# Performance work log

Hardware: AMD Instinct MI355X
Metric: run time of the kernel (lower is better)

Reference implementation:

```python
import jax, jax.numpy as jnp
import numpy as np

B, C, H, W = 8, 512, 32, 32
NH = 8
DH = C // NH
HW = H * W
LN_EPS = 1e-5
NORM_EPS = 1e-12  # torch F.normalize eps


def setup_inputs() -> dict:
    key = jax.random.key(0)
    ks = jax.random.split(key, 8)
    s = 0.02
    return {
        "x": jax.random.normal(ks[0], (B, C, H, W), dtype=jnp.float32),
        "qkv_w": jax.random.normal(ks[1], (3 * C, C), dtype=jnp.float32) * s,
        "proj_w": jax.random.normal(ks[2], (C, C), dtype=jnp.float32) * s,
        "proj_b": jnp.zeros((C,), dtype=jnp.float32),
        "temperature": jnp.ones((NH, 1, 1), dtype=jnp.float32),
        "ln_g": jnp.ones((C,), dtype=jnp.float32),
        "ln_b": jnp.zeros((C,), dtype=jnp.float32),
        "pos_embed": jax.random.normal(ks[3], (1, HW, C), dtype=jnp.float32) * s,
        "dw_w": jax.random.normal(ks[4], (C, 1, 3, 3), dtype=jnp.float32) * s,
        "dw_b": jnp.zeros((C,), dtype=jnp.float32),
        "pw_w": jax.random.normal(ks[5], (C, C, 1, 1), dtype=jnp.float32) * s,
        "pw_b": jnp.zeros((C,), dtype=jnp.float32),
    }


def _l2norm_tokens(t):
    # normalize along token axis (dim=-2), like F.normalize(t, dim=-2)
    n = jnp.sqrt(jnp.sum(t * t, axis=-2, keepdims=True))
    return t / jnp.maximum(n, NORM_EPS)


def _layernorm(t, g, b):
    mu = jnp.mean(t, axis=-1, keepdims=True)
    var = jnp.mean((t - mu) ** 2, axis=-1, keepdims=True)
    return (t - mu) * jax.lax.rsqrt(var + LN_EPS) * g + b


def _dsconv(t, dw_w, dw_b, pw_w, pw_b):
    # depthwise 3x3 SAME + pointwise 1x1, NCHW / OIHW
    y = jax.lax.conv_general_dilated(
        t, dw_w, window_strides=(1, 1), padding="SAME",
        dimension_numbers=("NCHW", "OIHW", "NCHW"), feature_group_count=C)
    y = y + dw_b[None, :, None, None]
    y = jax.lax.conv_general_dilated(
        y, pw_w, window_strides=(1, 1), padding="SAME",
        dimension_numbers=("NCHW", "OIHW", "NCHW"))
    return y + pw_b[None, :, None, None]


def reference(x, qkv_w, proj_w, proj_b, temperature, ln_g, ln_b, pos_embed, dw_w, dw_b, pw_w, pw_b):
    save = x
    t = jnp.transpose(x.reshape(B, C, HW), (0, 2, 1))  # [B, HW, C]
    t = t + pos_embed
    # qkv projection (no bias)
    qkv = t @ qkv_w.T  # [B, HW, 3C]
    qkv = qkv.reshape(B, HW, 3, NH, DH).transpose(2, 0, 3, 1, 4)  # [3,B,NH,HW,DH]
    q, k, v = qkv[0], qkv[1], qkv[2]
    q = _l2norm_tokens(q)
    k = _l2norm_tokens(k)
    attn = jnp.einsum("bhnd,bhmd->bhnm", q, k) * temperature[None]  # [B,NH,HW,HW]
    attn = jax.nn.softmax(attn, axis=-1)
    o = jnp.einsum("bhnm,bhmd->bhnd", attn, v)  # [B,NH,HW,DH]
    o = o.transpose(0, 2, 1, 3).reshape(B, HW, C)
    o = o @ proj_w.T + proj_b
    o = _layernorm(o, ln_g, ln_b)
    o = jnp.transpose(o, (0, 2, 1)).reshape(B, C, H, W)
    o = o + save
    return o + _dsconv(o, dw_w, dw_b, pw_w, pw_b)
```

## Files before the change

### kernel.cpp

```cpp
#include <hip/hip_runtime.h>
#include <math.h>

#define BB_ 8
#define C_ 512
#define C3_ 1536
#define HW_ 1024
#define NH_ 8
#define DH_ 64
#define HH_ 32
#define WW_ 32

typedef __attribute__((ext_vector_type(8))) short short8;
typedef __attribute__((ext_vector_type(4))) short short4v;
typedef __attribute__((ext_vector_type(8))) unsigned short ushort8;
typedef __attribute__((ext_vector_type(4))) unsigned short ushort4_t;
typedef __attribute__((ext_vector_type(4))) float f32x4;
typedef unsigned short ushort;

__device__ inline ushort f2bf(float f) {
  union { float f; unsigned u; } v;
  v.f = f;
  unsigned r = v.u + 0x7fffu + ((v.u >> 16) & 1u);
  return (ushort)(r >> 16);
}
__device__ inline float bf2f(ushort u) {
  union { unsigned u; float f; } v;
  v.u = ((unsigned)u) << 16;
  return v.f;
}

__device__ inline unsigned cvt_pk_bf16(float a, float b) {
  unsigned r;
  asm("v_cvt_pk_bf16_f32 %0, %1, %2" : "=v"(r) : "v"(a), "v"(b));
  return r;
}

__device__ inline float fast_exp2(float x) {
#if __has_builtin(__builtin_amdgcn_exp2f)
  return __builtin_amdgcn_exp2f(x);
#else
  return exp2f(x);
#endif
}

#define GLD16(gptr, lptr)                                                     \
  __builtin_amdgcn_global_load_lds(                                           \
      (const __attribute__((address_space(1))) unsigned int*)(gptr),          \
      (__attribute__((address_space(3))) unsigned int*)(lptr), 16, 0, 0)

__global__ __launch_bounds__(256) void prep_kernel(
    const float* __restrict__ x, const float* __restrict__ pos,
    const float* __restrict__ qkv_w, const float* __restrict__ proj_w,
    const float* __restrict__ pw_w, ushort* __restrict__ t,
    ushort* __restrict__ xT, ushort* __restrict__ wts,
    float* __restrict__ sums) {
  const int bid = blockIdx.x;
  const int tid = threadIdx.x;
  if (bid >= 2304) {
    sums[(bid - 2304) * 256 + tid] = 0.f;
    return;
  }
  if (bid >= 1024) {
    int i = ((bid - 1024) * 256 + tid) * 4;
    float4 v;
    if (i < 786432) v = *(const float4*)&qkv_w[i];
    else if (i < 1048576) v = *(const float4*)&proj_w[i - 786432];
    else v = *(const float4*)&pw_w[i - 1048576];
    union { unsigned u[2]; ushort4_t s; } o4;
    o4.u[0] = cvt_pk_bf16(v.x, v.y);
    o4.u[1] = cvt_pk_bf16(v.z, v.w);
    *(ushort4_t*)&wts[i] = o4.s;
    return;
  }
  __shared__ float tile[64][65];
  const int n0 = (bid & 15) * 64, c0 = ((bid >> 4) & 7) * 64, b = bid >> 7;
#pragma unroll
  for (int it = 0; it < 4; it++) {
    int c_l = (tid >> 4) + it * 16;
    int n_l4 = (tid & 15) * 4;
    float4 v = *(const float4*)&x[((size_t)(b * C_ + c0 + c_l)) * HW_ + n0 + n_l4];
    tile[c_l][n_l4 + 0] = v.x;
    tile[c_l][n_l4 + 1] = v.y;
    tile[c_l][n_l4 + 2] = v.z;
    tile[c_l][n_l4 + 3] = v.w;
  }
  __syncthreads();
#pragma unroll
  for (int it = 0; it < 4; it++) {
    int n_l = (tid >> 4) + it * 16;
    int c_l4 = (tid & 15) * 4;
    size_t token = (size_t)(b * HW_ + n0 + n_l);
    float4 pv = *(const float4*)&pos[(n0 + n_l) * C_ + c0 + c_l4];
    float xv0 = tile[c_l4 + 0][n_l], xv1 = tile[c_l4 + 1][n_l];
    float xv2 = tile[c_l4 + 2][n_l], xv3 = tile[c_l4 + 3][n_l];
    ushort4_t tb = {f2bf(xv0 + pv.x), f2bf(xv1 + pv.y), f2bf(xv2 + pv.z),
                    f2bf(xv3 + pv.w)};
    ushort4_t xb = {f2bf(xv0), f2bf(xv1), f2bf(xv2), f2bf(xv3)};
    *(ushort4_t*)&t[token * C_ + c0 + c_l4] = tb;
    *(ushort4_t*)&xT[token * C_ + c0 + c_l4] = xb;
  }
}

__global__ __launch_bounds__(256) void gemm_qkv(
    const ushort* __restrict__ A, const ushort* __restrict__ Wm,
    ushort* __restrict__ out, ushort* __restrict__ vt,
    float* __restrict__ qsum, float* __restrict__ ksum) {
  const int N = C3_, K = C_;
  __shared__ alignas(16) ushort smem[2 * 128 * 64];
  ushort* As = smem;
  ushort* Bs = smem + 128 * 64;
  const int f = blockIdx.y * gridDim.x + blockIdx.x;
  const int xcd = f & 7, idx = f >> 3;
  const int bm = (xcd * 8 + idx / 12) * 128;
  const int bn = (idx % 12) * 128;
  const int tid = threadIdx.x;
  const int w = tid >> 6, lane = tid & 63;
  const int wm = 64 * (w & 1), wn = 64 * (w >> 1);
  const int l15 = lane & 15, lq = lane >> 4;

  f32x4 acc[4][4];
#pragma unroll
  for (int i = 0; i < 4; i++)
#pragma unroll
    for (int j = 0; j < 4; j++) acc[i][j] = (f32x4){0.f, 0.f, 0.f, 0.f};

  const int srr8 = lane >> 3, sq3 = lane & 7;

  for (int k0 = 0; k0 < K; k0 += 64) {
    __syncthreads();
#pragma unroll
    for (int it = 0; it < 4; it++) {
      int r = w * 32 + it * 8 + srr8;
      int g = (sq3 - r) & 7;
      GLD16(A + (size_t)(bm + r) * K + k0 + g * 8, &As[(w * 32 + it * 8) * 64]);
      GLD16(Wm + (size_t)(bn + r) * K + k0 + g * 8, &Bs[(w * 32 + it * 8) * 64]);
    }
    __syncthreads();
#pragma unroll
    for (int kk = 0; kk < 2; kk++) {
      short8 af[4], bf[4];
#pragma unroll
      for (int nt = 0; nt < 4; nt++) {
        int r = wm + nt * 16 + l15;
        af[nt] = *(const short8*)&As[r * 64 + (((kk * 4 + lq) + r) & 7) * 8];
        int c = wn + nt * 16 + l15;
        bf[nt] = *(const short8*)&Bs[c * 64 + (((kk * 4 + lq) + c) & 7) * 8];
      }
#pragma unroll
      for (int i = 0; i < 4; i++)
#pragma unroll
        for (int j = 0; j < 4; j++)
          acc[i][j] = __builtin_amdgcn_mfma_f32_16x16x32_bf16(
              af[i], bf[j], acc[i][j], 0, 0, 0);
    }
  }

  const int b = bm >> 10;
  if (bn < 1024) {
    __syncthreads();
    ushort* T = smem;
#pragma unroll
    for (int j = 0; j < 4; j++) {
      int c_l = wn + j * 16 + l15;
      int c = bn + c_l;
      float ss = 0.f;
#pragma unroll
      for (int i = 0; i < 4; i++) {
#pragma unroll
        for (int r = 0; r < 4; r++) {
          int m_l = wm + i * 16 + lq * 4 + r;
          float v = acc[i][j][r];
          ss += v * v;
          T[m_l * 128 + (((c_l >> 3) ^ (m_l & 15)) << 3) + (c_l & 7)] =
              f2bf(v);
        }
      }
      ss += __shfl_xor(ss, 16);
      ss += __shfl_xor(ss, 32);
      if (lq == 0) {
        if (c < 512) atomicAdd(&qsum[b * 512 + c], ss);
        else atomicAdd(&ksum[b * 512 + c - 512], ss);
      }
    }
    __syncthreads();
    const int jj = tid & 15, mrow = tid >> 4;
#pragma unroll
    for (int p = 0; p < 8; p++) {
      int m_l = p * 16 + mrow;
      ushort8 v8 = *(const ushort8*)&T[m_l * 128 + ((jj ^ (m_l & 15)) << 3)];
      *(ushort8*)&out[(size_t)(bm + m_l) * N + bn + jj * 8] = v8;
    }
  } else {
    __syncthreads();
    ushort* T = smem;
#pragma unroll
    for (int j = 0; j < 4; j++) {
      int c_l = wn + j * 16 + l15;
#pragma unroll
      for (int i = 0; i < 4; i++) {
        int n_l = wm + i * 16 + lq * 4;
        union { unsigned u[2]; ushort4_t s; } pu;
        pu.u[0] = cvt_pk_bf16(acc[i][j][0], acc[i][j][1]);
        pu.u[1] = cvt_pk_bf16(acc[i][j][2], acc[i][j][3]);
        *(ushort4_t*)&T[c_l * 128 + (((n_l >> 3) ^ (c_l & 15)) << 3) +
                        (n_l & 7)] = pu.s;
      }
    }
    __syncthreads();
    const int jj = tid & 15, crow = tid >> 4;
    const int n0 = bm & 1023;
#pragma unroll
    for (int p = 0; p < 8; p++) {
      int c_l = p * 16 + crow;
      ushort8 v8 = *(const ushort8*)&T[c_l * 128 + ((jj ^ (c_l & 15)) << 3)];
      int hd = bn - 1024 + c_l;
      *(ushort8*)&vt[((size_t)(b * 512 + hd)) * HW_ + n0 + jj * 8] = v8;
    }
  }
}

template <int EPI>
__global__ __launch_bounds__(256) void gemm_n64(
    const ushort* __restrict__ A, const ushort* __restrict__ Wm,
    const float* __restrict__ bias, void* __restrict__ outv,
    const ushort* __restrict__ resid, int N, int K) {
  __shared__ alignas(16) ushort As[128 * 64];
  __shared__ alignas(16) ushort Bs[64 * 64];
  __shared__ alignas(16) float Cs[EPI == 2 ? 64 * 128 : 4];
  const int f = blockIdx.y * gridDim.x + blockIdx.x;
  const int xcd = f & 7, idx = f >> 3;
  const int nbx = gridDim.x;
  const int bm = (xcd * (gridDim.y >> 3) + idx / nbx) * 128;
  const int bn = (idx % nbx) * 64;
  const int tid = threadIdx.x;
  const int w = tid >> 6, lane = tid & 63;
  const int wm = 64 * (w & 1), wn = 32 * (w >> 1);
  const int l15 = lane & 15, lq = lane >> 4;

  f32x4 acc[4][2];
#pragma unroll
  for (int i = 0; i < 4; i++)
#pragma unroll
    for (int j = 0; j < 2; j++) acc[i][j] = (f32x4){0.f, 0.f, 0.f, 0.f};

  const int srr8 = lane >> 3, sq3 = lane & 7;

  for (int k0 = 0; k0 < K; k0 += 64) {
    __syncthreads();
#pragma unroll
    for (int it = 0; it < 4; it++) {
      int r = w * 32 + it * 8 + srr8;
      int g = (sq3 - r) & 7;
      GLD16(A + (size_t)(bm + r) * K + k0 + g * 8, &As[(w * 32 + it * 8) * 64]);
    }
#pragma unroll
    for (int it = 0; it < 2; it++) {
      int r = w * 16 + it * 8 + srr8;
      int g = (sq3 - r) & 7;
      GLD16(Wm + (size_t)(bn + r) * K + k0 + g * 8, &Bs[(w * 16 + it * 8) * 64]);
    }
    __syncthreads();
#pragma unroll
    for (int kk = 0; kk < 2; kk++) {
      short8 af[4], bf[2];
#pragma unroll
      for (int nt = 0; nt < 4; nt++) {
        int r = wm + nt * 16 + l15;
        af[nt] = *(const short8*)&As[r * 64 + (((kk * 4 + lq) + r) & 7) * 8];
      }
#pragma unroll
      for (int j = 0; j < 2; j++) {
        int c = wn + j * 16 + l15;
        bf[j] = *(const short8*)&Bs[c * 64 + (((kk * 4 + lq) + c) & 7) * 8];
      }
#pragma unroll
      for (int i = 0; i < 4; i++)
#pragma unroll
        for (int j = 0; j < 2; j++)
          acc[i][j] = __builtin_amdgcn_mfma_f32_16x16x32_bf16(
              af[i], bf[j], acc[i][j], 0, 0, 0);
    }
  }

  if (EPI == 1) {
#pragma unroll
    for (int i = 0; i < 4; i++) {
#pragma unroll
      for (int j = 0; j < 2; j++) {
        int c = bn + wn + j * 16 + l15;
        float bv = bias[c];
#pragma unroll
        for (int r = 0; r < 4; r++) {
          int m = bm + wm + i * 16 + lq * 4 + r;
          float v = acc[i][j][r] + bv;
          ((ushort*)outv)[(size_t)m * N + c] = f2bf(v);
        }
      }
    }
  } else {
#pragma unroll
    for (int i = 0; i < 4; i++) {
#pragma unroll
      for (int j = 0; j < 2; j++) {
        int c_l = wn + j * 16 + l15;
        int m_l = wm + i * 16 + lq * 4;
        float bv = bias[bn + c_l];
        f32x4 vv;
#pragma unroll
        for (int r = 0; r < 4; r++) {
          int m = bm + m_l + r;
          vv[r] = acc[i][j][r] + bv + bf2f(resid[(size_t)m * C_ + bn + c_l]);
        }
        int phys = (m_l >> 2) ^ (c_l & 31);
        *(f32x4*)&Cs[c_l * 128 + phys * 4] = vv;
      }
    }
    __syncthreads();
    const int b = bm >> 10, s0 = bm & (HW_ - 1);
    const int l5 = tid & 31;
    const int rr = tid >> 5;
    float* outp = (float*)outv;
#pragma unroll
    for (int pass = 0; pass < 8; pass++) {
      int row = rr + pass * 8;
      int phys = l5 ^ (row & 31);
      f32x4 vv = *(const f32x4*)&Cs[row * 128 + phys * 4];
      *(f32x4*)&outp[((size_t)(b * C_ + bn + row)) * HW_ + s0 + l5 * 4] = vv;
    }
  }
}

__global__ __launch_bounds__(256) void attn_mfma_kernel(
    const ushort* __restrict__ qkv, const ushort* __restrict__ vt,
    const float* __restrict__ qsum, const float* __restrict__ ksum,
    const float* __restrict__ temp, ushort* __restrict__ o) {
  __shared__ alignas(16) ushort Ks[2][64 * 64];
  __shared__ alignas(16) ushort Vts[2][64 * 64];
  __shared__ float sc_lds[64];

  const int tid = threadIdx.x;
  const int w = tid >> 6, lane = tid & 63;
  const int quad = lane >> 4, lcol = lane & 15;
  const int bh = blockIdx.x & 63;
  const int qt = blockIdx.x >> 6;
  const int b = bh >> 3, h = bh & 7;
  const int q0 = qt * 128;

  if (tid < 64) {
    float qs = qsum[b * 512 + h * 64 + tid];
    float ks = ksum[b * 512 + h * 64 + tid];
    float iq = 1.0f / fmaxf(sqrtf(qs), 1e-12f);
    float ik = 1.0f / fmaxf(sqrtf(ks), 1e-12f);
    sc_lds[tid] = iq * ik * temp[h] * 1.44269504088896340736f;
  }

  const ushort* kg = qkv + (size_t)b * HW_ * C3_ + C_ + h * 64;
  const ushort* vg = vt + (size_t)(bh * 64) * HW_;

  const int srow0 = tid >> 3;
  const int sc = tid & 7;

#pragma unroll
  for (int it = 0; it < 2; it++) {
    int row = srow0 + it * 32;
    int scg = sc ^ (row & 7);
    GLD16(kg + (size_t)row * C3_ + scg * 8, &Ks[0][w * 512 + it * 2048]);
    GLD16(vg + (size_t)row * HW_ + scg * 8, &Vts[0][w * 512 + it * 2048]);
  }
  __syncthreads();

  short8 qf[2][2];
#pragma unroll
  for (int qg = 0; qg < 2; qg++) {
    const int m = q0 + w * 32 + qg * 16 + lcol;
    const ushort* qrow = qkv + ((size_t)(b * HW_ + m)) * C3_ + h * 64;
#pragma unroll
    for (int kc = 0; kc < 2; kc++) {
      ushort8 q8 = *(const ushort8*)&qrow[kc * 32 + quad * 8];
      union { short8 v; ushort u[8]; } pk;
#pragma unroll
      for (int j = 0; j < 8; j++) {
        int d = kc * 32 + quad * 8 + j;
        pk.u[j] = f2bf(bf2f(q8[j]) * sc_lds[d]);
      }
      qf[qg][kc] = pk.v;
    }
  }

  f32x4 ot[2][4];
#pragma unroll
  for (int qg = 0; qg < 2; qg++)
#pragma unroll
    for (int dt = 0; dt < 4; dt++) ot[qg][dt] = (f32x4){0.f, 0.f, 0.f, 0.f};
  float lsum[2] = {0.f, 0.f};

  for (int kt = 0; kt < 16; kt++) {
    if (kt > 0) __syncthreads();
    const int cur = kt & 1;
    if (kt + 1 < 16) {
      const int nxt = cur ^ 1;
#pragma unroll
      for (int it = 0; it < 2; it++) {
        int row = srow0 + it * 32;
        int scg = sc ^ (row & 7);
        GLD16(kg + (size_t)((kt + 1) * 64 + row) * C3_ + scg * 8,
              &Ks[nxt][w * 512 + it * 2048]);
        GLD16(vg + (size_t)row * HW_ + (kt + 1) * 64 + scg * 8,
              &Vts[nxt][w * 512 + it * 2048]);
      }
    }

    f32x4 sfr[2][4];
#pragma unroll
    for (int qg = 0; qg < 2; qg++)
#pragma unroll
      for (int nt = 0; nt < 4; nt++) sfr[qg][nt] = (f32x4){0.f, 0.f, 0.f, 0.f};
#pragma unroll
    for (int kc = 0; kc < 2; kc++) {
#pragma unroll
      for (int nt = 0; nt < 4; nt++) {
        int row = nt * 16 + lcol;
        short8 kf = *(const short8*)
            &Ks[cur][row * 64 + (((kc * 4 + quad) ^ (row & 7)) * 8)];
        sfr[0][nt] = __builtin_amdgcn_mfma_f32_16x16x32_bf16(kf, qf[0][kc],
                                                             sfr[0][nt], 0, 0, 0);
        sfr[1][nt] = __builtin_amdgcn_mfma_f32_16x16x32_bf16(kf, qf[1][kc],
                                                             sfr[1][nt], 0, 0, 0);
      }
    }

    unsigned pu[2][4][2];
#pragma unroll
    for (int qg = 0; qg < 2; qg++) {
#pragma unroll
      for (int nt = 0; nt < 4; nt++) {
        float f0 = fast_exp2(sfr[qg][nt][0]);
        float f1 = fast_exp2(sfr[qg][nt][1]);
        float f2 = fast_exp2(sfr[qg][nt][2]);
        float f3 = fast_exp2(sfr[qg][nt][3]);
        lsum[qg] += f0 + f1 + f2 + f3;
        pu[qg][nt][0] = cvt_pk_bf16(f0, f1);
        pu[qg][nt][1] = cvt_pk_bf16(f2, f3);
      }
    }

#pragma unroll
    for (int ntp = 0; ntp < 2; ntp++) {
      union { unsigned u[4]; short8 v; } pf0, pf1;
      pf0.u[0] = pu[0][2 * ntp][0];
      pf0.u[1] = pu[0][2 * ntp][1];
      pf0.u[2] = pu[0][2 * ntp + 1][0];
      pf0.u[3] = pu[0][2 * ntp + 1][1];
      pf1.u[0] = pu[1][2 * ntp][0];
      pf1.u[1] = pu[1][2 * ntp][1];
      pf1.u[2] = pu[1][2 * ntp + 1][0];
      pf1.u[3] = pu[1][2 * ntp + 1][1];
      int key0 = (2 * ntp) * 16 + quad * 4;
      int key1 = (2 * ntp + 1) * 16 + quad * 4;
#pragma unroll
      for (int dt = 0; dt < 4; dt++) {
        int d = dt * 16 + lcol;
        short4v v0 = *(const short4v*)
            &Vts[cur][d * 64 + (((key0 >> 3) ^ (d & 7)) * 8) + (key0 & 7)];
        short4v v1 = *(const short4v*)
            &Vts[cur][d * 64 + (((key1 >> 3) ^ (d & 7)) * 8) + (key1 & 7)];
        short8 vf = {v0[0], v0[1], v0[2], v0[3], v1[0], v1[1], v1[2], v1[3]};
        ot[0][dt] = __builtin_amdgcn_mfma_f32_16x16x32_bf16(vf, pf0.v,
                                                            ot[0][dt], 0, 0, 0);
        ot[1][dt] = __builtin_amdgcn_mfma_f32_16x16x32_bf16(vf, pf1.v,
                                                            ot[1][dt], 0, 0, 0);
      }
    }
  }

#pragma unroll
  for (int qg = 0; qg < 2; qg++) {
    float s = lsum[qg];
    s += __shfl_xor(s, 16);
    s += __shfl_xor(s, 32);
    const float inv = 1.0f / s;
    const int m = q0 + w * 32 + qg * 16 + lcol;
    ushort* orow = o + ((size_t)(b * HW_ + m)) * C_ + h * 64;
#pragma unroll
    for (int dt = 0; dt < 4; dt++) {
      union { unsigned u[2]; ushort4_t s4; } pu2;
      pu2.u[0] = cvt_pk_bf16(ot[qg][dt][0] * inv, ot[qg][dt][1] * inv);
      pu2.u[1] = cvt_pk_bf16(ot[qg][dt][2] * inv, ot[qg][dt][3] * inv);
      *(ushort4_t*)&orow[dt * 16 + quad * 4] = pu2.s4;
    }
  }
}

__global__ __launch_bounds__(512) void gemm_proj_ln(
    const ushort* __restrict__ A, const ushort* __restrict__ Wm,
    const float* __restrict__ bias, const float* __restrict__ g,
    const float* __restrict__ bb, const ushort* __restrict__ resid,
    ushort* __restrict__ ybf) {
  __shared__ alignas(16) ushort As[2][16 * 32];
  __shared__ alignas(16) ushort Bs[2][512 * 32];
  __shared__ float red[8][16][2];
  const int bm = blockIdx.x * 16;
  const int tid = threadIdx.x;
  const int w = tid >> 6, lane = tid & 63;
  const int l15 = lane & 15, lq = lane >> 4;
  const int srr = lane >> 2, sq1 = lane & 3;

  f32x4 acc[4];
#pragma unroll
  for (int j = 0; j < 4; j++) acc[j] = (f32x4){0.f, 0.f, 0.f, 0.f};

  auto stage = [&](int kt, int bufi) {
#pragma unroll
    for (int it = 0; it < 4; it++) {
      int r = it * 128 + w * 16 + srr;
      int q = (sq1 - (r >> 1)) & 3;
      GLD16(Wm + (size_t)r * C_ + kt * 32 + q * 8,
            &Bs[bufi][(it * 128 + w * 16) * 32]);
    }
    if (w == 0) {
      int r = srr;
      int q = (sq1 - (r >> 1)) & 3;
      GLD16(A + (size_t)(bm + r) * C_ + kt * 32 + q * 8, &As[bufi][0]);
    }
  };

  stage(0, 0);

  for (int ks = 0; ks < 16; ks++) {
    __syncthreads();
    const int cur = ks & 1;
    if (ks + 1 < 16) stage(ks + 1, cur ^ 1);

    short8 af, bf[4];
    {
      int r = l15;
      af = *(const short8*)&As[cur][r * 32 + (((lq + (r >> 1)) & 3) * 8)];
    }
#pragma unroll
    for (int j = 0; j < 4; j++) {
      int c = w * 64 + j * 16 + l15;
      bf[j] = *(const short8*)&Bs[cur][c * 32 + (((lq + (c >> 1)) & 3) * 8)];
    }
#pragma unroll
    for (int j = 0; j < 4; j++)
      acc[j] = __builtin_amdgcn_mfma_f32_16x16x32_bf16(af, bf[j], acc[j],
                                                       0, 0, 0);
  }

  float bv[4];
#pragma unroll
  for (int j = 0; j < 4; j++) bv[j] = bias[w * 64 + j * 16 + l15];

  float s1v[4], s2v[4];
#pragma unroll
  for (int r = 0; r < 4; r++) {
    float a = 0.f, q2 = 0.f;
#pragma unroll
    for (int j = 0; j < 4; j++) {
      float v = acc[j][r] + bv[j];
      acc[j][r] = v;
      a += v;
      q2 += v * v;
    }
    s1v[r] = a;
    s2v[r] = q2;
  }
#pragma unroll
  for (int off = 1; off < 16; off <<= 1) {
#pragma unroll
    for (int r = 0; r < 4; r++) {
      s1v[r] += __shfl_xor(s1v[r], off);
      s2v[r] += __shfl_xor(s2v[r], off);
    }
  }
  if (l15 == 0) {
#pragma unroll
    for (int r = 0; r < 4; r++) {
      int tok = lq * 4 + r;
      red[w][tok][0] = s1v[r];
      red[w][tok][1] = s2v[r];
    }
  }
  __syncthreads();

  float gv[4], bbv[4];
#pragma unroll
  for (int j = 0; j < 4; j++) {
    gv[j] = g[w * 64 + j * 16 + l15];
    bbv[j] = bb[w * 64 + j * 16 + l15];
  }

  float* T = (float*)&Bs[0][0];
#pragma unroll
  for (int r = 0; r < 4; r++) {
    int tok = lq * 4 + r;
    float su = 0.f, sq = 0.f;
#pragma unroll
    for (int ww = 0; ww < 8; ww++) {
      su += red[ww][tok][0];
      sq += red[ww][tok][1];
    }
    float mu = su * (1.0f / C_);
    float var = sq * (1.0f / C_) - mu * mu;
    float rstd = rsqrtf(var + 1e-5f);
    int s = (tok << 3) | (tok & 7);
#pragma unroll
    for (int j = 0; j < 4; j++) {
      int c = w * 64 + j * 16 + l15;
      float y = (acc[j][r] - mu) * rstd * gv[j] + bbv[j];
      int q = c >> 2;
      T[tok * 512 + (((q ^ s) & 127) << 2) + (c & 3)] = y;
    }
  }
  __syncthreads();

  const int mrow = tid >> 5, j0 = tid & 31;
  const int s2 = (mrow << 3) | (mrow & 7);
#pragma unroll
  for (int p = 0; p < 2; p++) {
    int c0 = p * 256 + j0 * 8;
    int q0 = c0 >> 2;
    f32x4 a = *(const f32x4*)&T[mrow * 512 + (((q0 ^ s2) & 127) << 2)];
    f32x4 b2 = *(const f32x4*)&T[mrow * 512 + ((((q0 + 1) ^ s2) & 127) << 2)];
    int m = bm + mrow;
    ushort8 r8 = *(const ushort8*)&resid[(size_t)m * C_ + c0];
    union { unsigned u[4]; ushort8 v; } pk;
    pk.u[0] = cvt_pk_bf16(a[0] + bf2f(r8[0]), a[1] + bf2f(r8[1]));
    pk.u[1] = cvt_pk_bf16(a[2] + bf2f(r8[2]), a[3] + bf2f(r8[3]));
    pk.u[2] = cvt_pk_bf16(b2[0] + bf2f(r8[4]), b2[1] + bf2f(r8[5]));
    pk.u[3] = cvt_pk_bf16(b2[2] + bf2f(r8[6]), b2[3] + bf2f(r8[7]));
    *(ushort8*)&ybf[(size_t)m * C_ + c0] = pk.v;
  }
}

__global__ __launch_bounds__(256) void dwconv_kernel(
    const ushort* __restrict__ y, const float* __restrict__ w,
    const float* __restrict__ bias, ushort* __restrict__ out) {
  const int cg = threadIdx.x & 63, tg = threadIdx.x >> 6;
  const int c0 = cg * 8;
  float wreg[9][8], breg[8];
#pragma unroll
  for (int j = 0; j < 8; j++) {
    breg[j] = bias[c0 + j];
#pragma unroll
    for (int kk = 0; kk < 9; kk++) wreg[kk][j] = w[(c0 + j) * 9 + kk];
  }
  const int base = blockIdx.x * 16 + tg * 4;
  const int b = base >> 10, s = base & (HW_ - 1);
  const int hh = s >> 5, w0 = s & 31;
  float acc[4][8];
#pragma unroll
  for (int i = 0; i < 4; i++)
#pragma unroll
    for (int j = 0; j < 8; j++) acc[i][j] = breg[j];
#pragma unroll
  for (int ky = 0; ky < 3; ky++) {
    int yy = hh + ky - 1;
    if (yy < 0 || yy >= HH_) continue;
    const ushort* yrow = &y[((size_t)(b * HW_ + yy * 32)) * C_ + c0];
#pragma unroll
    for (int xx6 = 0; xx6 < 6; xx6++) {
      int xx = w0 - 1 + xx6;
      if (xx < 0 || xx >= WW_) continue;
      ushort8 v8 = *(const ushort8*)&yrow[(size_t)xx * C_];
      float vf[8];
#pragma unroll
      for (int j = 0; j < 8; j++) vf[j] = bf2f(v8[j]);
#pragma unroll
      for (int i = 0; i < 4; i++) {
        int kx = xx6 - i;
        if (kx < 0 || kx > 2) continue;
        const float* wk = wreg[ky * 3 + kx];
#pragma unroll
        for (int j = 0; j < 8; j++) acc[i][j] += wk[j] * vf[j];
      }
    }
  }
#pragma unroll
  for (int i = 0; i < 4; i++) {
    union { unsigned u[4]; ushort8 v; } pku;
    pku.u[0] = cvt_pk_bf16(acc[i][0], acc[i][1]);
    pku.u[1] = cvt_pk_bf16(acc[i][2], acc[i][3]);
    pku.u[2] = cvt_pk_bf16(acc[i][4], acc[i][5]);
    pku.u[3] = cvt_pk_bf16(acc[i][6], acc[i][7]);
    *(ushort8*)&out[(size_t)(base + i) * C_ + c0] = pku.v;
  }
}

extern "C" void kernel_launch(void* const* d_in, const int* in_sizes, int n_in,
                              void* d_out, int out_size, void* d_ws,
                              size_t ws_size, hipStream_t stream) {
  const float* x = (const float*)d_in[0];
  const float* qkv_w = (const float*)d_in[1];
  const float* proj_w = (const float*)d_in[2];
  const float* proj_b = (const float*)d_in[3];
  const float* temperature = (const float*)d_in[4];
  const float* ln_g = (const float*)d_in[5];
  const float* ln_b = (const float*)d_in[6];
  const float* pos = (const float*)d_in[7];
  const float* dw_w = (const float*)d_in[8];
  const float* dw_b = (const float*)d_in[9];
  const float* pw_w = (const float*)d_in[10];
  const float* pw_b = (const float*)d_in[11];
  float* out = (float*)d_out;

  float* ws = (float*)d_ws;
  ushort* qkv_bf = (ushort*)ws;
  ushort* t_bf = (ushort*)(ws + (size_t)6 * 1024 * 1024);
  ushort* xT_bf = (ushort*)(ws + (size_t)12 * 1024 * 1024);
  ushort* wts = (ushort*)(ws + (size_t)14 * 1024 * 1024);
  ushort* qkvw_bf = wts;
  ushort* projw_bf = wts + 786432;
  ushort* pww_bf = wts + 1048576;
  float* sums = ws + (size_t)15 * 1024 * 1024;
  float* qsum = sums;
  float* ksum = sums + 4096;
  ushort* vtb = (ushort*)(ws + (size_t)16 * 1024 * 1024);

  const int M = BB_ * HW_;

  prep_kernel<<<2336, 256, 0, stream>>>(x, pos, qkv_w, proj_w, pw_w, t_bf,
                                        xT_bf, wts, sums);
  gemm_qkv<<<dim3(C3_ / 128, M / 128), 256, 0, stream>>>(
      t_bf, qkvw_bf, qkv_bf, vtb, qsum, ksum);
  attn_mfma_kernel<<<BB_ * NH_ * (HW_ / 128), 256, 0, stream>>>(
      qkv_bf, vtb, qsum, ksum, temperature, t_bf);
  gemm_proj_ln<<<M / 16, 512, 0, stream>>>(t_bf, projw_bf, proj_b, ln_g,
                                           ln_b, xT_bf, xT_bf);
  dwconv_kernel<<<M / 16, 256, 0, stream>>>(xT_bf, dw_w, dw_b, t_bf);
  gemm_n64<2><<<dim3(C_ / 64, M / 128), 256, 0, stream>>>(
      t_bf, pww_bf, pw_b, out, xT_bf, C_, C_);
}
```

Baseline: 187.5 us.

## Split fused proj+LayerNorm into tiled GEMM plus separate LN-residual kernel

After: 182.4 us, median of 3. -2.7%, faster.

```diff
diff --git a/kernel.cpp b/kernel.cpp
--- a/kernel.cpp
+++ b/kernel.cpp
@@ -226,7 +226,7 @@
     const ushort* __restrict__ resid, int N, int K) {
   __shared__ alignas(16) ushort As[128 * 64];
   __shared__ alignas(16) ushort Bs[64 * 64];
-  __shared__ alignas(16) float Cs[EPI == 2 ? 64 * 128 : 4];
+  __shared__ alignas(16) float Cs[EPI == 2 ? 64 * 128 : 64 * 64];
   const int f = blockIdx.y * gridDim.x + blockIdx.x;
   const int xcd = f & 7, idx = f >> 3;
   const int nbx = gridDim.x;
@@ -283,19 +283,28 @@
   }
 
   if (EPI == 1) {
+    ushort* Tc = (ushort*)Cs;
 #pragma unroll
     for (int i = 0; i < 4; i++) {
 #pragma unroll
       for (int j = 0; j < 2; j++) {
-        int c = bn + wn + j * 16 + l15;
-        float bv = bias[c];
+        int c_l = wn + j * 16 + l15;
+        float bv = bias[bn + c_l];
 #pragma unroll
         for (int r = 0; r < 4; r++) {
-          int m = bm + wm + i * 16 + lq * 4 + r;
-          float v = acc[i][j][r] + bv;
-          ((ushort*)outv)[(size_t)m * N + c] = f2bf(v);
+          int m_l = wm + i * 16 + lq * 4 + r;
+          Tc[m_l * 64 + (((c_l >> 3) ^ (m_l & 7)) << 3) + (c_l & 7)] =
+              f2bf(acc[i][j][r] + bv);
         }
       }
+    }
+    __syncthreads();
+    const int jj = tid & 7, mrow = tid >> 3;
+#pragma unroll
+    for (int p = 0; p < 4; p++) {
+      int m_l = p * 32 + mrow;
+      ushort8 v8 = *(const ushort8*)&Tc[m_l * 64 + ((jj ^ (m_l & 7)) << 3)];
+      *(ushort8*)&((ushort*)outv)[(size_t)(bm + m_l) * N + bn + jj * 8] = v8;
     }
   } else {
 #pragma unroll
@@ -491,146 +500,45 @@
   }
 }
 
-__global__ __launch_bounds__(512) void gemm_proj_ln(
-    const ushort* __restrict__ A, const ushort* __restrict__ Wm,
-    const float* __restrict__ bias, const float* __restrict__ g,
-    const float* __restrict__ bb, const ushort* __restrict__ resid,
-    ushort* __restrict__ ybf) {
-  __shared__ alignas(16) ushort As[2][16 * 32];
-  __shared__ alignas(16) ushort Bs[2][512 * 32];
-  __shared__ float red[8][16][2];
-  const int bm = blockIdx.x * 16;
-  const int tid = threadIdx.x;
-  const int w = tid >> 6, lane = tid & 63;
-  const int l15 = lane & 15, lq = lane >> 4;
-  const int srr = lane >> 2, sq1 = lane & 3;
-
-  f32x4 acc[4];
-#pragma unroll
-  for (int j = 0; j < 4; j++) acc[j] = (f32x4){0.f, 0.f, 0.f, 0.f};
-
-  auto stage = [&](int kt, int bufi) {
-#pragma unroll
-    for (int it = 0; it < 4; it++) {
-      int r = it * 128 + w * 16 + srr;
-      int q = (sq1 - (r >> 1)) & 3;
-      GLD16(Wm + (size_t)r * C_ + kt * 32 + q * 8,
-            &Bs[bufi][(it * 128 + w * 16) * 32]);
-    }
-    if (w == 0) {
-      int r = srr;
-      int q = (sq1 - (r >> 1)) & 3;
-      GLD16(A + (size_t)(bm + r) * C_ + kt * 32 + q * 8, &As[bufi][0]);
-    }
-  };
-
-  stage(0, 0);
-
-  for (int ks = 0; ks < 16; ks++) {
-    __syncthreads();
-    const int cur = ks & 1;
-    if (ks + 1 < 16) stage(ks + 1, cur ^ 1);
-
-    short8 af, bf[4];
-    {
-      int r = l15;
-      af = *(const short8*)&As[cur][r * 32 + (((lq + (r >> 1)) & 3) * 8)];
-    }
-#pragma unroll
-    for (int j = 0; j < 4; j++) {
-      int c = w * 64 + j * 16 + l15;
-      bf[j] = *(const short8*)&Bs[cur][c * 32 + (((lq + (c >> 1)) & 3) * 8)];
-    }
-#pragma unroll
-    for (int j = 0; j < 4; j++)
-      acc[j] = __builtin_amdgcn_mfma_f32_16x16x32_bf16(af, bf[j], acc[j],
-                                                       0, 0, 0);
-  }
-
-  float bv[4];
-#pragma unroll
-  for (int j = 0; j < 4; j++) bv[j] = bias[w * 64 + j * 16 + l15];
-
-  float s1v[4], s2v[4];
-#pragma unroll
-  for (int r = 0; r < 4; r++) {
-    float a = 0.f, q2 = 0.f;
-#pragma unroll
-    for (int j = 0; j < 4; j++) {
-      float v = acc[j][r] + bv[j];
-      acc[j][r] = v;
-      a += v;
-      q2 += v * v;
-    }
-    s1v[r] = a;
-    s2v[r] = q2;
-  }
-#pragma unroll
-  for (int off = 1; off < 16; off <<= 1) {
-#pragma unroll
-    for (int r = 0; r < 4; r++) {
-      s1v[r] += __shfl_xor(s1v[r], off);
-      s2v[r] += __shfl_xor(s2v[r], off);
-    }
-  }
-  if (l15 == 0) {
-#pragma unroll
-    for (int r = 0; r < 4; r++) {
-      int tok = lq * 4 + r;
-      red[w][tok][0] = s1v[r];
-      red[w][tok][1] = s2v[r];
-    }
-  }
-  __syncthreads();
-
-  float gv[4], bbv[4];
-#pragma unroll
-  for (int j = 0; j < 4; j++) {
-    gv[j] = g[w * 64 + j * 16 + l15];
-    bbv[j] = bb[w * 64 + j * 16 + l15];
-  }
-
-  float* T = (float*)&Bs[0][0];
-#pragma unroll
-  for (int r = 0; r < 4; r++) {
-    int tok = lq * 4 + r;
-    float su = 0.f, sq = 0.f;
-#pragma unroll
-    for (int ww = 0; ww < 8; ww++) {
-      su += red[ww][tok][0];
-      sq += red[ww][tok][1];
-    }
-    float mu = su * (1.0f / C_);
-    float var = sq * (1.0f / C_) - mu * mu;
-    float rstd = rsqrtf(var + 1e-5f);
-    int s = (tok << 3) | (tok & 7);
-#pragma unroll
-    for (int j = 0; j < 4; j++) {
-      int c = w * 64 + j * 16 + l15;
-      float y = (acc[j][r] - mu) * rstd * gv[j] + bbv[j];
-      int q = c >> 2;
-      T[tok * 512 + (((q ^ s) & 127) << 2) + (c & 3)] = y;
-    }
-  }
-  __syncthreads();
-
-  const int mrow = tid >> 5, j0 = tid & 31;
-  const int s2 = (mrow << 3) | (mrow & 7);
-#pragma unroll
-  for (int p = 0; p < 2; p++) {
-    int c0 = p * 256 + j0 * 8;
-    int q0 = c0 >> 2;
-    f32x4 a = *(const f32x4*)&T[mrow * 512 + (((q0 ^ s2) & 127) << 2)];
-    f32x4 b2 = *(const f32x4*)&T[mrow * 512 + ((((q0 + 1) ^ s2) & 127) << 2)];
-    int m = bm + mrow;
-    ushort8 r8 = *(const ushort8*)&resid[(size_t)m * C_ + c0];
-    union { unsigned u[4]; ushort8 v; } pk;
-    pk.u[0] = cvt_pk_bf16(a[0] + bf2f(r8[0]), a[1] + bf2f(r8[1]));
-    pk.u[1] = cvt_pk_bf16(a[2] + bf2f(r8[2]), a[3] + bf2f(r8[3]));
-    pk.u[2] = cvt_pk_bf16(b2[0] + bf2f(r8[4]), b2[1] + bf2f(r8[5]));
-    pk.u[3] = cvt_pk_bf16(b2[2] + bf2f(r8[6]), b2[3] + bf2f(r8[7]));
-    *(ushort8*)&ybf[(size_t)m * C_ + c0] = pk.v;
-  }
+__global__ __launch_bounds__(256) void ln_residual_kernel(
+    const ushort* __restrict__ po, const ushort* xT,
+    const float* __restrict__ g, const float* __restrict__ bb, ushort* ybf) {
+  const int wv = threadIdx.x >> 6, lane = threadIdx.x & 63;
+  const int token = blockIdx.x * 4 + wv;
+  const int c0 = lane * 8;
+  ushort8 p8 = *(const ushort8*)&po[(size_t)token * C_ + c0];
+  float v[8];
+  float s = 0.f;
+#pragma unroll
+  for (int j = 0; j < 8; j++) {
+    v[j] = bf2f(p8[j]);
+    s += v[j];
+  }
+#pragma unroll
+  for (int off = 32; off; off >>= 1) s += __shfl_xor(s, off);
+  float mu = s * (1.0f / C_);
+  float vs = 0.f;
+#pragma unroll
+  for (int j = 0; j < 8; j++) {
+    v[j] -= mu;
+    vs += v[j] * v[j];
+  }
+#pragma unroll
+  for (int off = 32; off; off >>= 1) vs += __shfl_xor(vs, off);
+  float rstd = rsqrtf(vs * (1.0f / C_) + 1e-5f);
+  float4 g0 = *(const float4*)&g[c0], g1 = *(const float4*)&g[c0 + 4];
+  float4 b0 = *(const float4*)&bb[c0], b1 = *(const float4*)&bb[c0 + 4];
+  ushort8 r8 = *(const ushort8*)&xT[(size_t)token * C_ + c0];
+  float gg[8] = {g0.x, g0.y, g0.z, g0.w, g1.x, g1.y, g1.z, g1.w};
+  float bbv[8] = {b0.x, b0.y, b0.z, b0.w, b1.x, b1.y, b1.z, b1.w};
+  union { unsigned u[4]; ushort8 v; } pk;
+#pragma unroll
+  for (int j = 0; j < 4; j++)
+    pk.u[j] = cvt_pk_bf16(v[2 * j] * rstd * gg[2 * j] + bbv[2 * j] +
+                              bf2f(r8[2 * j]),
+                          v[2 * j + 1] * rstd * gg[2 * j + 1] +
+                              bbv[2 * j + 1] + bf2f(r8[2 * j + 1]));
+  *(ushort8*)&ybf[(size_t)token * C_ + c0] = pk.v;
 }
 
 __global__ __launch_bounds__(256) void dwconv_kernel(
@@ -707,6 +615,7 @@
   float* ws = (float*)d_ws;
   ushort* qkv_bf = (ushort*)ws;
   ushort* t_bf = (ushort*)(ws + (size_t)6 * 1024 * 1024);
+  ushort* proj_bf = (ushort*)(ws + (size_t)8 * 1024 * 1024);
   ushort* xT_bf = (ushort*)(ws + (size_t)12 * 1024 * 1024);
   ushort* wts = (ushort*)(ws + (size_t)14 * 1024 * 1024);
   ushort* qkvw_bf = wts;
@@ -725,8 +634,10 @@
       t_bf, qkvw_bf, qkv_bf, vtb, qsum, ksum);
   attn_mfma_kernel<<<BB_ * NH_ * (HW_ / 128), 256, 0, stream>>>(
       qkv_bf, vtb, qsum, ksum, temperature, t_bf);
-  gemm_proj_ln<<<M / 16, 512, 0, stream>>>(t_bf, projw_bf, proj_b, ln_g,
-                                           ln_b, xT_bf, xT_bf);
+  gemm_n64<1><<<dim3(C_ / 64, M / 128), 256, 0, stream>>>(
+      t_bf, projw_bf, proj_b, proj_bf, nullptr, C_, C_);
+  ln_residual_kernel<<<M / 4, 256, 0, stream>>>(proj_bf, xT_bf, ln_g, ln_b,
+                                                xT_bf);
   dwconv_kernel<<<M / 16, 256, 0, stream>>>(xT_bf, dw_w, dw_b, t_bf);
   gemm_n64<2><<<dim3(C_ / 64, M / 128), 256, 0, stream>>>(
       t_bf, pww_bf, pw_b, out, xT_bf, C_, C_);
```
